# Kernel tuning notes

Hardware: AMD Instinct MI355X
Metric: run time of the kernel (lower is better)

Reference implementation:

```python
import jax, jax.numpy as jnp
import numpy as np
import math

B, DIM, H, W = 4, 96, 64, 64
DIM3 = DIM * 3
DSTATE = 16

def _dwconv(x, w, b):
    # x: (B, d, L); torch Conv1d(k=4, pad=3, groups=d) then slice [:L] == left-pad 3
    y = jax.lax.conv_general_dilated(x, w, (1,), [(3, 0)],
                                     dimension_numbers=('NCH', 'OIH', 'NCH'),
                                     feature_group_count=x.shape[1])
    return y + b[None, :, None]

def _ln(x, g, b):
    m = jnp.mean(x, -1, keepdims=True)
    v = jnp.var(x, -1, keepdims=True)
    return (x - m) * jax.lax.rsqrt(v + 1e-5) * g + b

def _selective_scan(u, delta, A, Bs, Cs, D, z, delta_bias):
    # u, delta, z: (B, d, L); A: (d, N); Bs, Cs: (B, N, L)
    delta = jax.nn.softplus(delta + delta_bias[None, :, None])
    dT, uT = jnp.moveaxis(delta, 2, 0), jnp.moveaxis(u, 2, 0)   # (L, B, d)
    BT, CT = jnp.moveaxis(Bs, 2, 0), jnp.moveaxis(Cs, 2, 0)     # (L, B, N)
    h0 = jnp.zeros((u.shape[0], A.shape[0], A.shape[1]), u.dtype)
    def step(h, inp):
        d_t, u_t, b_t, c_t = inp
        h = jnp.exp(d_t[..., None] * A) * h + (d_t * u_t)[..., None] * b_t[:, None, :]
        return h, jnp.einsum('bdn,bn->bd', h, c_t)
    _, ys = jax.lax.scan(step, h0, (dT, uT, BT, CT))
    y = jnp.moveaxis(ys, 0, 2) + D[None, :, None] * u
    return y * jax.nn.silu(z)

def _sss(x, z_anchor, in_w, conv_w, conv_b, x_w, dt_w, dt_b, Alog, Dp, out_w):
    Bb, C, Hh, Ww = x.shape
    L = Hh * Ww
    r = dt_w.shape[0]
    xf = x.reshape(Bb, C, L).transpose(0, 2, 1) + z_anchor[:, None, :]
    x_in, z_gate = jnp.split(xf @ in_w, 2, axis=-1)
    xc = jax.nn.silu(_dwconv(x_in.transpose(0, 2, 1), conv_w, conv_b))  # (B, di, L)
    xdbl = xc.transpose(0, 2, 1) @ x_w
    dt, Bs, Cs = jnp.split(xdbl, [r, r + DSTATE], axis=-1)
    y = _selective_scan(xc, (dt @ dt_w).transpose(0, 2, 1), -jnp.exp(Alog),
                        Bs.transpose(0, 2, 1), Cs.transpose(0, 2, 1), Dp,
                        z_gate.transpose(0, 2, 1), dt_b)
    return (y.transpose(0, 2, 1) @ out_w).transpose(0, 2, 1).reshape(Bb, C, Hh, Ww)

def _sts(x, K, Q, in_w, conv_w, conv_b, kln_g, kln_b, k_w, k_b, qln_g, qln_b, q_w, q_b,
         dtbc_w, dt_w, dt_b, gate_w, gate_b, Alog, Dp, out_w):
    Bb, C, Hh, Ww = x.shape
    L = Hh * Ww
    r = dt_w.shape[0]
    xf = x.reshape(Bb, C, L).transpose(0, 2, 1)
    xc = jax.nn.silu(_dwconv((xf @ in_w).transpose(0, 2, 1), conv_w, conv_b))  # (B, di, L)
    x_t = xc.transpose(0, 2, 1)
    Kf = K.reshape(Bb, C, L).transpose(0, 2, 1)
    Qf = Q.reshape(Bb, C, L).transpose(0, 2, 1)
    K_p = jax.nn.silu(_ln(Kf, kln_g, kln_b) @ k_w + k_b)
    Q_p = jax.nn.silu(_ln(Qf, qln_g, qln_b) @ q_w + q_b)
    xdbl = jnp.concatenate([x_t, K_p], -1) @ dtbc_w
    dt, Bs, Cs = jnp.split(xdbl, [r, r + DSTATE], axis=-1)
    z_g = (jnp.concatenate([x_t, Q_p], -1) @ gate_w + gate_b).transpose(0, 2, 1)
    y = _selective_scan(xc, (dt @ dt_w).transpose(0, 2, 1), -jnp.exp(Alog),
                        Bs.transpose(0, 2, 1), Cs.transpose(0, 2, 1), Dp, z_g, dt_b)
    return (y.transpose(0, 2, 1) @ out_w).transpose(0, 2, 1).reshape(Bb, C, Hh, Ww)

def setup_inputs():
    key = jax.random.key(0)
    ks = iter(jax.random.split(key, 64))
    def nrm(shape, s=0.02):
        return jax.random.normal(next(ks), shape, jnp.float32) * s
    di, di3 = DIM * 2, DIM3 * 2
    r, r3 = math.ceil(DIM / 16), math.ceil(DIM3 / 16)
    Alog = jnp.log(jnp.tile(jnp.arange(1.0, DSTATE + 1.0, dtype=jnp.float32), (di, 1)))
    Alog3 = jnp.log(jnp.tile(jnp.arange(1.0, DSTATE + 1.0, dtype=jnp.float32), (di3, 1)))
    return dict(
        m_ll=jax.random.normal(next(ks), (B, DIM, H, W), jnp.float32),
        m_high=jax.random.normal(next(ks), (B, DIM3, H, W), jnp.float32),
        z=jax.random.normal(next(ks), (B, DIM), jnp.float32),
        K=jax.random.normal(next(ks), (B, DIM3, H, W), jnp.float32),
        Q=jax.random.normal(next(ks), (B, DIM3, H, W), jnp.float32),
        s_in_w=nrm((DIM, 2 * di)), s_conv_w=nrm((di, 1, 4), 0.2), s_conv_b=nrm((di,)),
        s_x_w=nrm((di, r + 2 * DSTATE)), s_dt_w=nrm((r, di)), s_dt_b=nrm((di,)),
        s_Alog=Alog, s_D=jnp.ones((di,), jnp.float32), s_out_w=nrm((di, DIM)),
        t_in_w=nrm((DIM3, di3)), t_conv_w=nrm((di3, 1, 4), 0.2), t_conv_b=nrm((di3,)),
        t_kln_g=jnp.ones((DIM3,), jnp.float32), t_kln_b=jnp.zeros((DIM3,), jnp.float32),
        t_k_w=nrm((DIM3, di3)), t_k_b=nrm((di3,)),
        t_qln_g=jnp.ones((DIM3,), jnp.float32), t_qln_b=jnp.zeros((DIM3,), jnp.float32),
        t_q_w=nrm((DIM3, di3)), t_q_b=nrm((di3,)),
        t_dtbc_w=nrm((2 * di3, r3 + 2 * DSTATE)), t_dt_w=nrm((r3, di3)), t_dt_b=nrm((di3,)),
        t_gate_w=nrm((2 * di3, di3)), t_gate_b=nrm((di3,)),
        t_Alog=Alog3, t_D=jnp.ones((di3,), jnp.float32), t_out_w=nrm((di3, DIM3)),
    )

def reference(m_ll, m_high, z, K, Q,
              s_in_w, s_conv_w, s_conv_b, s_x_w, s_dt_w, s_dt_b, s_Alog, s_D, s_out_w,
              t_in_w, t_conv_w, t_conv_b, t_kln_g, t_kln_b, t_k_w, t_k_b,
              t_qln_g, t_qln_b, t_q_w, t_q_b, t_dtbc_w, t_dt_w, t_dt_b,
              t_gate_w, t_gate_b, t_Alog, t_D, t_out_w):
    o1 = m_ll + _sss(m_ll, z, s_in_w, s_conv_w, s_conv_b, s_x_w, s_dt_w, s_dt_b, s_Alog, s_D, s_out_w)
    o2 = m_high + _sts(m_high, K, Q, t_in_w, t_conv_w, t_conv_b, t_kln_g, t_kln_b, t_k_w, t_k_b,
                       t_qln_g, t_qln_b, t_q_w, t_q_b, t_dtbc_w, t_dt_w, t_dt_b,
                       t_gate_w, t_gate_b, t_Alog, t_D, t_out_w)
    return (o1, o2)
```

## Files before the change

kernel.cpp:

```cpp
#include <hip/hip_runtime.h>
#include <math.h>

#define L 4096

typedef unsigned short u16;
typedef unsigned int u32;
typedef float f32x4 __attribute__((ext_vector_type(4)));
typedef short s16x8 __attribute__((ext_vector_type(8)));
typedef __attribute__((address_space(3))) unsigned int lds_u32;
typedef __attribute__((address_space(1))) unsigned int glb_u32;

__device__ __forceinline__ float softplus_f(float x) {
  return fmaxf(x, 0.f) + log1pf(__expf(-fabsf(x)));
}
__device__ __forceinline__ float silu_f(float x) {
  return x / (1.f + __expf(-x));
}
__device__ __forceinline__ float bf2f(u16 v) {
  return __uint_as_float(((unsigned)v) << 16);
}
__device__ __forceinline__ u16 f2bf(float f) {
  unsigned u = __float_as_uint(f);
  u += 0x7FFFu + ((u >> 16) & 1u);
  return (u16)(u >> 16);
}

struct WSeg { const float* src; u16* dst; int K, N, Npad; };
struct WAll { WSeg s[9]; };

__global__ __launch_bounds__(256) void wconv_k(WAll wa) {
  const WSeg w = wa.s[blockIdx.z];
  const int nb = blockIdx.x * 32, kb = blockIdx.y * 32;
  if (nb >= w.Npad || kb >= w.K) return;
  __shared__ float t[32][33];
  const int tx = threadIdx.x & 31, ty = threadIdx.x >> 5;
  for (int r = ty; r < 32; r += 8) {
    int k = kb + r, n = nb + tx;
    t[r][tx] = (n < w.N) ? w.src[(size_t)k * w.N + n] : 0.f;
  }
  __syncthreads();
  for (int r = ty; r < 32; r += 8) {
    int n = nb + r;
    w.dst[(size_t)n * w.K + kb + tx] = f2bf(t[tx][r]);
  }
}

struct TSeg { const float *x, *gam, *bet, *bias2; u16* out; int C, doLN; };
struct TPack { TSeg s[4]; };

__global__ __launch_bounds__(256) void trans_pack_k(TPack pk) {
  const TSeg t = pk.s[blockIdx.x >> 9];
  const int local = blockIdx.x & 511;
  const int C = t.C;
  __shared__ float tile[288][33];
  __shared__ float psum[8][32], psq[8][32];
  __shared__ float mm[32], rr[32];
  const int tid = threadIdx.x;
  const int l0 = (local & 127) * 32;
  const int b = local >> 7;
  const int lane32 = tid & 31, row8 = tid >> 5;
  const float* xb = t.x + (size_t)b * C * L + l0;

  for (int c = row8; c < C; c += 8)
    tile[c][lane32] = xb[(size_t)c * L + lane32];
  __syncthreads();

  if (t.doLN) {
    float s = 0.f, sq = 0.f;
    for (int c = row8; c < C; c += 8) {
      float v = tile[c][lane32];
      s += v; sq = fmaf(v, v, sq);
    }
    psum[row8][lane32] = s; psq[row8][lane32] = sq;
    __syncthreads();
    if (row8 == 0) {
      float ts = 0.f, tq = 0.f;
      #pragma unroll
      for (int g = 0; g < 8; ++g) { ts += psum[g][lane32]; tq += psq[g][lane32]; }
      float m = ts / C;
      float var = tq / C - m * m;
      mm[lane32] = m;
      rr[lane32] = rsqrtf(var + 1e-5f);
    }
    __syncthreads();
  }

  u16* ob = t.out + ((size_t)b * L + l0) * C;
  const int total = 32 * C;
  for (int o = tid * 8; o < total; o += 2048) {
    int tt = o / C, c = o % C;
    float m = 0.f, rs = 0.f;
    if (t.doLN) { m = mm[tt]; rs = rr[tt]; }
    union { u16 u[8]; int4 v; } pkv;
    #pragma unroll
    for (int j = 0; j < 8; ++j) {
      float v = tile[c + j][tt];
      if (t.doLN) v = (v - m) * rs * t.gam[c + j] + t.bet[c + j];
      else if (t.bias2) v += t.bias2[b * C + c + j];
      pkv.u[j] = f2bf(v);
    }
    *(int4*)(ob + o) = pkv.v;
  }
}

struct CSeg { const u16* x; const float* w; const float* b; u16* y; int C, nbx; };
struct CPack { CSeg s[2]; int start1; };

__global__ __launch_bounds__(256) void conv_pack_k(CPack pk) {
  const int bid = blockIdx.x;
  const int si = bid >= pk.start1;
  const CSeg q = pk.s[si];
  const int local = si ? bid - pk.start1 : bid;
  const int C = q.C;
  const int c = (local % q.nbx) * 64 + (threadIdx.x & 63);
  const int chunk = (local / q.nbx) * 4 + (threadIdx.x >> 6);
  const int T0 = chunk * 8;
  const float w0 = q.w[c * 4], w1 = q.w[c * 4 + 1], w2 = q.w[c * 4 + 2], w3 = q.w[c * 4 + 3];
  const float bs = q.b[c];
  const bool first = (T0 & (L - 1)) == 0;
  float v[11];
  #pragma unroll
  for (int i = 0; i < 11; ++i) {
    if (i < 3 && first) v[i] = 0.f;
    else v[i] = bf2f(q.x[(size_t)(T0 - 3 + i) * C + c]);
  }
  #pragma unroll
  for (int j = 0; j < 8; ++j) {
    float s = bs + w0 * v[j] + w1 * v[j + 1] + w2 * v[j + 2] + w3 * v[j + 3];
    q.y[(size_t)(T0 + j) * C + c] = f2bf(silu_f(s));
  }
}

struct MSeg {
  const u16 *A0, *A1, *Wt;
  const float *bias, *res;
  float* outF; u16 *outB0, *outB1;
  int K, K1, Nout, ldA, ldo, split, nbx, nwg, epi;
};
struct MPack { MSeg s[4]; int starts[4]; int nseg; };

__global__ __launch_bounds__(256) void mfma_pack_k(MPack pk) {
  const int bid = blockIdx.x;
  int si = 0;
  #pragma unroll
  for (int k = 1; k < 4; ++k)
    if (k < pk.nseg && bid >= pk.starts[k]) si = k;
  const MSeg p = pk.s[si];
  const int wg = bid - pk.starts[si];

  __shared__ u16 As[2][4096];
  __shared__ u16 Bs[2][4096];
  const int tid = threadIdx.x;
  const int lane = tid & 63;
  const int wid = tid >> 6;
  const int wm = wid >> 1, wn = wid & 1;
  const int newid = (wg & 7) * (p.nwg >> 3) + (wg >> 3);
  const int n0 = (newid % p.nbx) * 128;
  const int m0 = (newid / p.nbx) * 128;
  const int srow = tid & 127;
  const int skc = tid >> 7;
  const int kgrp = lane >> 4, l16 = lane & 15;

  f32x4 acc[4][4];
  #pragma unroll
  for (int i = 0; i < 4; ++i)
    #pragma unroll
    for (int j = 0; j < 4; ++j)
      acc[i][j] = (f32x4){0.f, 0.f, 0.f, 0.f};

  auto stage = [&](int bi, int k0) {
    const u16* Ab = p.A0;
    int kc = k0;
    if (p.A1 && k0 >= p.K1) { Ab = p.A1; kc = k0 - p.K1; }
    const u16* g0 = Ab + (size_t)(m0 + srow) * p.ldA + kc + skc * 8;
    u16* Ad = &As[bi][0];
    __builtin_amdgcn_global_load_lds((const glb_u32*)g0,
        (lds_u32*)(Ad + wid * 512), 16, 0, 0);
    __builtin_amdgcn_global_load_lds((const glb_u32*)(g0 + 16),
        (lds_u32*)(Ad + 2048 + wid * 512), 16, 0, 0);
    const u16* h0 = p.Wt + (size_t)(n0 + srow) * p.K + k0 + skc * 8;
    u16* Bd = &Bs[bi][0];
    __builtin_amdgcn_global_load_lds((const glb_u32*)h0,
        (lds_u32*)(Bd + wid * 512), 16, 0, 0);
    __builtin_amdgcn_global_load_lds((const glb_u32*)(h0 + 16),
        (lds_u32*)(Bd + 2048 + wid * 512), 16, 0, 0);
  };

  const int nt = p.K >> 5;
  stage(0, 0);
  __syncthreads();
  for (int t = 0; t < nt; ++t) {
    const int cur = t & 1;
    if (t + 1 < nt) stage(cur ^ 1, (t + 1) << 5);
    s16x8 af[4], bfr[4];
    #pragma unroll
    for (int mi = 0; mi < 4; ++mi)
      af[mi] = *(const s16x8*)(&As[cur][0] + kgrp * 1024 + (wm * 64 + mi * 16 + l16) * 8);
    #pragma unroll
    for (int ni = 0; ni < 4; ++ni)
      bfr[ni] = *(const s16x8*)(&Bs[cur][0] + kgrp * 1024 + (wn * 64 + ni * 16 + l16) * 8);
    #pragma unroll
    for (int mi = 0; mi < 4; ++mi)
      #pragma unroll
      for (int ni = 0; ni < 4; ++ni)
        acc[mi][ni] = __builtin_amdgcn_mfma_f32_16x16x32_bf16(af[mi], bfr[ni], acc[mi][ni], 0, 0, 0);
    if (t + 1 < nt) __syncthreads();
  }

  if (p.epi == 2) {
    #pragma unroll
    for (int mi = 0; mi < 4; ++mi) {
      int token = m0 + wm * 64 + mi * 16 + (lane >> 4) * 4;
      int b = token >> 12, l = token & (L - 1);
      #pragma unroll
      for (int ni = 0; ni < 4; ++ni) {
        int n = n0 + wn * 64 + ni * 16 + l16;
        if (n < p.Nout) {
          size_t o = ((size_t)b * p.Nout + n) * L + l;
          float4 r = *(const float4*)(p.res + o);
          float4 v = make_float4(acc[mi][ni][0] + r.x, acc[mi][ni][1] + r.y,
                                 acc[mi][ni][2] + r.z, acc[mi][ni][3] + r.w);
          *(float4*)(p.outF + o) = v;
        }
      }
    }
  } else {
    #pragma unroll
    for (int mi = 0; mi < 4; ++mi) {
      #pragma unroll
      for (int j = 0; j < 4; ++j) {
        int token = m0 + wm * 64 + mi * 16 + (lane >> 4) * 4 + j;
        #pragma unroll
        for (int ni = 0; ni < 4; ++ni) {
          int n = n0 + wn * 64 + ni * 16 + l16;
          float v = acc[mi][ni][j];
          if (p.epi == 0) {
            if (n < p.Nout) p.outF[(size_t)token * p.ldo + n] = v;
          } else if (p.epi == 1) {
            if (n < p.Nout) p.outB0[(size_t)token * p.ldo + n] = f2bf(v);
          } else if (p.epi == 3) {
            if (n < p.Nout) p.outB0[(size_t)token * p.ldo + n] = f2bf(silu_f(v + p.bias[n]));
          } else if (p.epi == 4) {
            if (n < p.Nout) p.outB0[(size_t)token * p.ldo + n] = f2bf(v + p.bias[n]);
          } else {
            if (n < p.split) p.outB0[(size_t)token * p.split + n] = f2bf(v);
            else p.outB1[(size_t)token * p.split + (n - p.split)] = f2bf(v);
          }
        }
      }
    }
  }
}

struct FSeg { const float* A0; const float* W; const float* eb; float* out; int K, N, lda, ldo, nbx; };
struct FPack { FSeg s[2]; int start1; };

__global__ __launch_bounds__(256) void gemm_f32_pack_k(FPack pk) {
  const int bid = blockIdx.x;
  const int si = bid >= pk.start1;
  const FSeg p = pk.s[si];
  const int local = si ? bid - pk.start1 : bid;
  const int n0 = (local % p.nbx) * 64;
  const int m0 = (local / p.nbx) * 64;

  __shared__ __align__(16) float As[16][64];
  __shared__ __align__(16) float Bs[16][64];
  const int tid = threadIdx.x;
  const int kidx = tid >> 4;
  const int li4 = (tid & 15) << 2;
  const int r0 = (tid & 15) << 2;
  const int c0 = (tid >> 4) << 2;
  float acc[4][4] = {};

  for (int k0 = 0; k0 < p.K; k0 += 16) {
    __syncthreads();
    {
      const int row = tid >> 2;
      const int kk4 = (tid & 3) << 2;
      const float* src = p.A0 + (size_t)(m0 + row) * p.lda;
      #pragma unroll
      for (int j = 0; j < 4; ++j) {
        int k = k0 + kk4 + j;
        As[kk4 + j][row] = (k < p.K) ? src[k] : 0.f;
      }
    }
    {
      int k = k0 + kidx;
      #pragma unroll
      for (int j = 0; j < 4; ++j) {
        int n = n0 + li4 + j;
        Bs[kidx][li4 + j] = (k < p.K && n < p.N) ? p.W[(size_t)k * p.N + n] : 0.f;
      }
    }
    __syncthreads();
    #pragma unroll
    for (int kk = 0; kk < 16; ++kk) {
      float4 a = *(const float4*)&As[kk][r0];
      float4 bq = *(const float4*)&Bs[kk][c0];
      float av[4] = {a.x, a.y, a.z, a.w};
      float bv[4] = {bq.x, bq.y, bq.z, bq.w};
      #pragma unroll
      for (int i = 0; i < 4; ++i)
        #pragma unroll
        for (int j = 0; j < 4; ++j)
          acc[i][j] = fmaf(av[i], bv[j], acc[i][j]);
    }
  }
  float eb[4] = {p.eb[n0 + c0], p.eb[n0 + c0 + 1], p.eb[n0 + c0 + 2], p.eb[n0 + c0 + 3]};
  #pragma unroll
  for (int i = 0; i < 4; ++i) {
    float4 v;
    v.x = softplus_f(acc[i][0] + eb[0]);
    v.y = softplus_f(acc[i][1] + eb[1]);
    v.z = softplus_f(acc[i][2] + eb[2]);
    v.w = softplus_f(acc[i][3] + eb[3]);
    *(float4*)&p.out[(size_t)(m0 + r0 + i) * p.ldo + n0 + c0] = v;
  }
}

struct S2Seg {
  const u16* u; const float* dlt; const float* Alog; const float* xdbl;
  const float* Dp; const u16* zT; float* PF; u16* yT;
  int roff, Dch, CLen, NCH;
};
struct S2Pack { S2Seg s[2]; int start1; };

template<int PASS>
__global__ __launch_bounds__(256) void scan2_pack_k(S2Pack pk) {
  const int bid = blockIdx.x;
  const int si = bid >= pk.start1;
  const S2Seg q = pk.s[si];
  const int lbid = si ? bid - pk.start1 : bid;
  const int gtid = lbid * 256 + (int)threadIdx.x;
  const int Dch = q.Dch;
  const int npair = Dch >> 1;
  const int NC = L / q.CLen;
  const int dpi = gtid % npair;
  const int c = (gtid / npair) % NC;
  const int b = gtid / (npair * NC);
  const int d0 = dpi * 2;
  const size_t tok0 = (size_t)b * L + (size_t)c * q.CLen;

  float An[2][16], h[2][16];
  #pragma unroll
  for (int j = 0; j < 2; ++j)
    #pragma unroll
    for (int n = 0; n < 16; ++n) {
      An[j][n] = -__expf(q.Alog[(d0 + j) * 16 + n]);
      h[j][n] = 0.f;
    }
  bool fast = true;
  #pragma unroll
  for (int j = 0; j < 2; ++j)
    #pragma unroll
    for (int n = 1; n < 16; ++n) {
      float ref = (float)(n + 1) * An[j][0];
      if (fabsf(An[j][n] - ref) > 1e-4f * fabsf(ref)) fast = false;
    }

  const int ch0 = b * Dch + d0;
  if (PASS == 3) {
    #pragma unroll
    for (int j = 0; j < 2; ++j)
      #pragma unroll
      for (int n = 0; n < 16; ++n)
        h[j][n] = q.PF[((size_t)c * 32 + 16 + n) * q.NCH + ch0 + j];
  }
  const float Dd0 = q.Dp[d0], Dd1 = q.Dp[d0 + 1];
  const u16* up = q.u + tok0 * Dch + d0;
  const float* dp = q.dlt + tok0 * Dch + d0;
  const u16* zp = q.zT + tok0 * Dch + d0;
  u16* yr = q.yT + tok0 * Dch + d0;
  const float* xr = q.xdbl + tok0 * 64 + q.roff;
  float S0 = 0.f, S1 = 0.f;

  #define SCAN_BODY(FAST)                                                      \
  for (int t = 0; t < q.CLen; ++t) {                                           \
    const size_t od = (size_t)t * Dch;                                         \
    float2 dl2 = *(const float2*)(dp + od);                                    \
    u32 uu2 = *(const u32*)(up + od);                                          \
    float u0 = bf2f((u16)uu2), u1 = bf2f((u16)(uu2 >> 16));                    \
    float w0 = dl2.x * u0, w1 = dl2.y * u1;                                    \
    const float2* bp = (const float2*)(xr + (size_t)t * 64);                   \
    float Bv[16];                                                              \
    _Pragma("unroll")                                                          \
    for (int qq = 0; qq < 8; ++qq) {                                           \
      float2 bv = bp[qq]; Bv[2 * qq] = bv.x; Bv[2 * qq + 1] = bv.y;            \
    }                                                                          \
    if (PASS == 1) { S0 += dl2.x; S1 += dl2.y; }                               \
    float y0 = 0.f, y1 = 0.f;                                                  \
    if (FAST) {                                                                \
      float a0 = __expf(dl2.x * An[0][0]);                                     \
      float a1 = __expf(dl2.y * An[1][0]);                                     \
      float e0 = a0, e1 = a1;                                                  \
      h[0][0] = fmaf(e0, h[0][0], w0 * Bv[0]);                                 \
      h[1][0] = fmaf(e1, h[1][0], w1 * Bv[0]);                                 \
      _Pragma("unroll")                                                        \
      for (int n = 1; n < 16; ++n) {                                           \
        e0 *= a0; e1 *= a1;                                                    \
        h[0][n] = fmaf(e0, h[0][n], w0 * Bv[n]);                               \
        h[1][n] = fmaf(e1, h[1][n], w1 * Bv[n]);                               \
      }                                                                        \
    } else {                                                                   \
      _Pragma("unroll")                                                        \
      for (int n = 0; n < 16; ++n) {                                           \
        h[0][n] = fmaf(__expf(dl2.x * An[0][n]), h[0][n], w0 * Bv[n]);         \
        h[1][n] = fmaf(__expf(dl2.y * An[1][n]), h[1][n], w1 * Bv[n]);         \
      }                                                                        \
    }                                                                          \
    if (PASS == 3) {                                                           \
      _Pragma("unroll")                                                        \
      for (int qq = 0; qq < 8; ++qq) {                                         \
        float2 cv = bp[qq + 8];                                                \
        y0 = fmaf(h[0][2 * qq], cv.x, y0); y0 = fmaf(h[0][2 * qq + 1], cv.y, y0); \
        y1 = fmaf(h[1][2 * qq], cv.x, y1); y1 = fmaf(h[1][2 * qq + 1], cv.y, y1); \
      }                                                                        \
      u32 zz2 = *(const u32*)(zp + od);                                        \
      float z0 = bf2f((u16)zz2), z1 = bf2f((u16)(zz2 >> 16));                  \
      y0 = (y0 + Dd0 * u0) * silu_f(z0);                                       \
      y1 = (y1 + Dd1 * u1) * silu_f(z1);                                       \
      u32 out = (u32)f2bf(y0) | ((u32)f2bf(y1) << 16);                         \
      *(u32*)(yr + od) = out;                                                  \
    }                                                                          \
  }

  if (fast) { SCAN_BODY(1) } else { SCAN_BODY(0) }
  #undef SCAN_BODY

  if (PASS == 1) {
    #pragma unroll
    for (int n = 0; n < 16; ++n) {
      q.PF[((size_t)c * 32 + n) * q.NCH + ch0]     = __expf(An[0][n] * S0);
      q.PF[((size_t)c * 32 + n) * q.NCH + ch0 + 1] = __expf(An[1][n] * S1);
      q.PF[((size_t)c * 32 + 16 + n) * q.NCH + ch0]     = h[0][n];
      q.PF[((size_t)c * 32 + 16 + n) * q.NCH + ch0 + 1] = h[1][n];
    }
  }
}

__global__ __launch_bounds__(256) void stitch_pack_k(
    float* PF0, int NC0, int NCH0, int tot0,
    float* PF1, int NC1, int NCH1, int tot1) {
  int idx = blockIdx.x * 256 + threadIdx.x;
  float* PF; int NC, NCH;
  if (idx < tot0) { PF = PF0; NC = NC0; NCH = NCH0; }
  else { idx -= tot0; if (idx >= tot1) return; PF = PF1; NC = NC1; NCH = NCH1; }
  int ch = idx % NCH, n = idx / NCH;
  float hin = 0.f;
  for (int c = 0; c < NC; ++c) {
    float* Ps = PF + ((size_t)c * 32 + n) * NCH + ch;
    float* Fs = PF + ((size_t)c * 32 + 16 + n) * NCH + ch;
    float Pv = *Ps, Fv = *Fs;
    *Fs = hin;
    hin = fmaf(Pv, hin, Fv);
  }
}

extern "C" void kernel_launch(void* const* d_in, const int* in_sizes, int n_in,
                              void* d_out, int out_size, void* d_ws, size_t ws_size,
                              hipStream_t stream) {
  const float* m_ll    = (const float*)d_in[0];
  const float* m_high  = (const float*)d_in[1];
  const float* zanc    = (const float*)d_in[2];
  const float* Kin     = (const float*)d_in[3];
  const float* Qin     = (const float*)d_in[4];
  const float* s_in_w  = (const float*)d_in[5];
  const float* s_conv_w= (const float*)d_in[6];
  const float* s_conv_b= (const float*)d_in[7];
  const float* s_x_w   = (const float*)d_in[8];
  const float* s_dt_w  = (const float*)d_in[9];
  const float* s_dt_b  = (const float*)d_in[10];
  const float* s_Alog  = (const float*)d_in[11];
  const float* s_D     = (const float*)d_in[12];
  const float* s_out_w = (const float*)d_in[13];
  const float* t_in_w  = (const float*)d_in[14];
  const float* t_conv_w= (const float*)d_in[15];
  const float* t_conv_b= (const float*)d_in[16];
  const float* t_kln_g = (const float*)d_in[17];
  const float* t_kln_b = (const float*)d_in[18];
  const float* t_k_w   = (const float*)d_in[19];
  const float* t_k_b   = (const float*)d_in[20];
  const float* t_qln_g = (const float*)d_in[21];
  const float* t_qln_b = (const float*)d_in[22];
  const float* t_q_w   = (const float*)d_in[23];
  const float* t_q_b   = (const float*)d_in[24];
  const float* t_dtbc_w= (const float*)d_in[25];
  const float* t_dt_w  = (const float*)d_in[26];
  const float* t_dt_b  = (const float*)d_in[27];
  const float* t_gate_w= (const float*)d_in[28];
  const float* t_gate_b= (const float*)d_in[29];
  const float* t_Alog  = (const float*)d_in[30];
  const float* t_D     = (const float*)d_in[31];
  const float* t_out_w = (const float*)d_in[32];

  float* out1 = (float*)d_out;
  float* out2 = out1 + (size_t)4 * 96 * L;
  float* ws = (float*)d_ws;

  u16* w_sin   = (u16*)(ws + 0);
  u16* w_sx    = (u16*)(ws + 18432);
  u16* w_sout  = (u16*)(ws + 30720);
  u16* w_tin   = (u16*)(ws + 43008);
  u16* w_tk    = (u16*)(ws + 135168);
  u16* w_tq    = (u16*)(ws + 227328);
  u16* w_tdtbc = (u16*)(ws + 319488);
  u16* w_tgate = (u16*)(ws + 393216);
  u16* w_tout  = (u16*)(ws + 761856);

  float* B_ahi  = ws + 872448;
  float* B_aK   = ws + 2052096;
  float* B_aQ   = ws + 3231744;
  float* B_all  = ws + 4411392;
  float* B_xin  = ws + 5197824;
  float* B_zTs  = ws + 6770688;
  float* B_xc   = ws + 8343552;
  float* B_xin3 = ws + 9916416;
  float* B_xc3  = ws + 14635008;
  float* B_kp   = ws + 19353600;
  float* B_qp   = ws + 24072192;
  float* B_zg3  = ws + 28790784;
  float* B_xdbl = ws + 33509376;
  float* B_xdbl3= ws + 34557952;
  float* B_PFs  = ws + 35606528;
  float* B_dlt  = B_ahi;
  float* B_dlt3 = B_kp;
  u16* y_bf = (u16*)B_xin;
  u16* y3   = (u16*)B_xin3;
  float* PFt = out2;

  dim3 blk(256);

  {
    WAll wa;
    wa.s[0] = {s_in_w,   w_sin,    96, 384, 384};
    wa.s[1] = {s_x_w,    w_sx,    192,  38, 128};
    wa.s[2] = {s_out_w,  w_sout,  192,  96, 128};
    wa.s[3] = {t_in_w,   w_tin,   288, 576, 640};
    wa.s[4] = {t_k_w,    w_tk,    288, 576, 640};
    wa.s[5] = {t_q_w,    w_tq,    288, 576, 640};
    wa.s[6] = {t_dtbc_w, w_tdtbc, 1152, 50, 128};
    wa.s[7] = {t_gate_w, w_tgate, 1152, 576, 640};
    wa.s[8] = {t_out_w,  w_tout,  576, 288, 384};
    wconv_k<<<dim3(20, 36, 9), blk, 0, stream>>>(wa);
  }

  {
    TPack tp{};
    tp.s[0] = {m_ll,   nullptr, nullptr, zanc,    (u16*)B_all, 96,  0};
    tp.s[1] = {m_high, nullptr, nullptr, nullptr, (u16*)B_ahi, 288, 0};
    tp.s[2] = {Kin,    t_kln_g, t_kln_b, nullptr, (u16*)B_aK,  288, 1};
    tp.s[3] = {Qin,    t_qln_g, t_qln_b, nullptr, (u16*)B_aQ,  288, 1};
    trans_pack_k<<<dim3(2048), blk, 0, stream>>>(tp);
  }

  {
    MPack pk{}; pk.nseg = 4;
    pk.starts[0] = 0; pk.starts[1] = 384; pk.starts[2] = 1024; pk.starts[3] = 1664;
    MSeg a{}; a.A0 = (u16*)B_all; a.Wt = w_sin; a.K = 96; a.K1 = 1 << 28; a.Nout = 384;
    a.ldA = 96; a.split = 192; a.outB0 = (u16*)B_xin; a.outB1 = (u16*)B_zTs;
    a.nbx = 3; a.nwg = 384; a.epi = 5; pk.s[0] = a;
    MSeg b{}; b.A0 = (u16*)B_ahi; b.Wt = w_tin; b.K = 288; b.K1 = 1 << 28; b.Nout = 576;
    b.ldA = 288; b.ldo = 576; b.outB0 = (u16*)B_xin3; b.nbx = 5; b.nwg = 640; b.epi = 1; pk.s[1] = b;
    MSeg c{}; c.A0 = (u16*)B_aK; c.Wt = w_tk; c.K = 288; c.K1 = 1 << 28; c.Nout = 576;
    c.ldA = 288; c.ldo = 576; c.bias = t_k_b; c.outB0 = (u16*)B_kp; c.nbx = 5; c.nwg = 640; c.epi = 3; pk.s[2] = c;
    MSeg d{}; d.A0 = (u16*)B_aQ; d.Wt = w_tq; d.K = 288; d.K1 = 1 << 28; d.Nout = 576;
    d.ldA = 288; d.ldo = 576; d.bias = t_q_b; d.outB0 = (u16*)B_qp; d.nbx = 5; d.nwg = 640; d.epi = 3; pk.s[3] = d;
    mfma_pack_k<<<dim3(2304), blk, 0, stream>>>(pk);
  }

  {
    CPack cp{}; cp.start1 = 1536;
    cp.s[0] = {(u16*)B_xin,  s_conv_w, s_conv_b, (u16*)B_xc,  192, 3};
    cp.s[1] = {(u16*)B_xin3, t_conv_w, t_conv_b, (u16*)B_xc3, 576, 9};
    conv_pack_k<<<dim3(6144), blk, 0, stream>>>(cp);
  }

  {
    MPack pk{}; pk.nseg = 3;
    pk.starts[0] = 0; pk.starts[1] = 128; pk.starts[2] = 256; pk.starts[3] = 896;
    MSeg a{}; a.A0 = (u16*)B_xc; a.Wt = w_sx; a.K = 192; a.K1 = 1 << 28; a.Nout = 64;
    a.ldA = 192; a.ldo = 64; a.outF = B_xdbl; a.nbx = 1; a.nwg = 128; a.epi = 0; pk.s[0] = a;
    MSeg b{}; b.A0 = (u16*)B_xc3; b.A1 = (u16*)B_kp; b.Wt = w_tdtbc; b.K = 1152; b.K1 = 576;
    b.Nout = 64; b.ldA = 576; b.ldo = 64; b.outF = B_xdbl3; b.nbx = 1; b.nwg = 128; b.epi = 0; pk.s[1] = b;
    MSeg c{}; c.A0 = (u16*)B_xc3; c.A1 = (u16*)B_qp; c.Wt = w_tgate; c.K = 1152; c.K1 = 576;
    c.Nout = 576; c.ldA = 576; c.ldo = 576; c.bias = t_gate_b; c.outB0 = (u16*)B_zg3;
    c.nbx = 5; c.nwg = 640; c.epi = 4; pk.s[2] = c;
    mfma_pack_k<<<dim3(896), blk, 0, stream>>>(pk);
  }

  {
    FPack fp{}; fp.start1 = 768;
    fp.s[0] = {B_xdbl,  s_dt_w, s_dt_b, B_dlt,  6,  192, 64, 192, 3};
    fp.s[1] = {B_xdbl3, t_dt_w, t_dt_b, B_dlt3, 18, 576, 64, 576, 9};
    gemm_f32_pack_k<<<dim3(3072), blk, 0, stream>>>(fp);
  }

  S2Pack sp{}; sp.start1 = 192;
  sp.s[0] = {(u16*)B_xc,  B_dlt,  s_Alog, B_xdbl,  s_D, (u16*)B_zTs, B_PFs, y_bf, 6,  192, 32, 768};
  sp.s[1] = {(u16*)B_xc3, B_dlt3, t_Alog, B_xdbl3, t_D, (u16*)B_zg3, PFt,   y3,   18, 576, 64, 2304};
  scan2_pack_k<1><<<dim3(480), blk, 0, stream>>>(sp);
  stitch_pack_k<<<dim3(192), blk, 0, stream>>>(B_PFs, 128, 768, 12288, PFt, 64, 2304, 36864);
  scan2_pack_k<3><<<dim3(480), blk, 0, stream>>>(sp);

  {
    MPack pk{}; pk.nseg = 2;
    pk.starts[0] = 0; pk.starts[1] = 128; pk.starts[2] = 512; pk.starts[3] = 512;
    MSeg a{}; a.A0 = y_bf; a.Wt = w_sout; a.K = 192; a.K1 = 1 << 28; a.Nout = 96;
    a.ldA = 192; a.res = m_ll; a.outF = out1; a.nbx = 1; a.nwg = 128; a.epi = 2; pk.s[0] = a;
    MSeg b{}; b.A0 = y3; b.Wt = w_tout; b.K = 576; b.K1 = 1 << 28; b.Nout = 288;
    b.ldA = 576; b.res = m_high; b.outF = out2; b.nbx = 3; b.nwg = 384; b.epi = 2; pk.s[1] = b;
    mfma_pack_k<<<dim3(512), blk, 0, stream>>>(pk);
  }
}
```

Measured before the change: 428.8 us.

## Scan one channel per thread, stage bf16 GEMM epilogue via swizzled LDS, split weight conversion

The selective-scan kernels now assign one channel per thread instead of two, doubling the grid so more waves are in flight while cutting per-thread register state. The MFMA GEMM's bf16 epilogues now write the tile into a swizzled shared-memory buffer, then emit 16-byte vectorized global stores instead of scattered 2-byte stores. The weight-conversion launch is split so the out-projection segment runs with a smaller grid. The tradeoffs are narrower per-thread loads in the scan and extra barriers plus LDS traffic in the epilogue.

```diff
diff --git a/kernel.cpp b/kernel.cpp
--- a/kernel.cpp
+++ b/kernel.cpp
@@ -26,7 +26,7 @@
 }
 
 struct WSeg { const float* src; u16* dst; int K, N, Npad; };
-struct WAll { WSeg s[9]; };
+struct WAll { WSeg s[8]; };
 
 __global__ __launch_bounds__(256) void wconv_k(WAll wa) {
   const WSeg w = wa.s[blockIdx.z];
@@ -148,8 +148,9 @@
   const MSeg p = pk.s[si];
   const int wg = bid - pk.starts[si];
 
-  __shared__ u16 As[2][4096];
-  __shared__ u16 Bs[2][4096];
+  __shared__ u16 lds[16384];
+  u16* As0 = lds;
+  u16* Bs0 = lds + 8192;
   const int tid = threadIdx.x;
   const int lane = tid & 63;
   const int wid = tid >> 6;
@@ -173,13 +174,13 @@
     int kc = k0;
     if (p.A1 && k0 >= p.K1) { Ab = p.A1; kc = k0 - p.K1; }
     const u16* g0 = Ab + (size_t)(m0 + srow) * p.ldA + kc + skc * 8;
-    u16* Ad = &As[bi][0];
+    u16* Ad = As0 + bi * 4096;
     __builtin_amdgcn_global_load_lds((const glb_u32*)g0,
         (lds_u32*)(Ad + wid * 512), 16, 0, 0);
     __builtin_amdgcn_global_load_lds((const glb_u32*)(g0 + 16),
         (lds_u32*)(Ad + 2048 + wid * 512), 16, 0, 0);
     const u16* h0 = p.Wt + (size_t)(n0 + srow) * p.K + k0 + skc * 8;
-    u16* Bd = &Bs[bi][0];
+    u16* Bd = Bs0 + bi * 4096;
     __builtin_amdgcn_global_load_lds((const glb_u32*)h0,
         (lds_u32*)(Bd + wid * 512), 16, 0, 0);
     __builtin_amdgcn_global_load_lds((const glb_u32*)(h0 + 16),
@@ -195,10 +196,10 @@
     s16x8 af[4], bfr[4];
     #pragma unroll
     for (int mi = 0; mi < 4; ++mi)
-      af[mi] = *(const s16x8*)(&As[cur][0] + kgrp * 1024 + (wm * 64 + mi * 16 + l16) * 8);
+      af[mi] = *(const s16x8*)(As0 + cur * 4096 + kgrp * 1024 + (wm * 64 + mi * 16 + l16) * 8);
     #pragma unroll
     for (int ni = 0; ni < 4; ++ni)
-      bfr[ni] = *(const s16x8*)(&Bs[cur][0] + kgrp * 1024 + (wn * 64 + ni * 16 + l16) * 8);
+      bfr[ni] = *(const s16x8*)(Bs0 + cur * 4096 + kgrp * 1024 + (wn * 64 + ni * 16 + l16) * 8);
     #pragma unroll
     for (int mi = 0; mi < 4; ++mi)
       #pragma unroll
@@ -207,7 +208,20 @@
     if (t + 1 < nt) __syncthreads();
   }
 
-  if (p.epi == 2) {
+  if (p.epi == 0) {
+    #pragma unroll
+    for (int mi = 0; mi < 4; ++mi) {
+      #pragma unroll
+      for (int j = 0; j < 4; ++j) {
+        int token = m0 + wm * 64 + mi * 16 + (lane >> 4) * 4 + j;
+        #pragma unroll
+        for (int ni = 0; ni < 4; ++ni) {
+          int n = n0 + wn * 64 + ni * 16 + l16;
+          if (n < p.Nout) p.outF[(size_t)token * p.ldo + n] = acc[mi][ni][j];
+        }
+      }
+    }
+  } else if (p.epi == 2) {
     #pragma unroll
     for (int mi = 0; mi < 4; ++mi) {
       int token = m0 + wm * 64 + mi * 16 + (lane >> 4) * 4;
@@ -225,27 +239,41 @@
       }
     }
   } else {
+    __syncthreads();
     #pragma unroll
     for (int mi = 0; mi < 4; ++mi) {
       #pragma unroll
       for (int j = 0; j < 4; ++j) {
-        int token = m0 + wm * 64 + mi * 16 + (lane >> 4) * 4 + j;
+        int tok = wm * 64 + mi * 16 + (lane >> 4) * 4 + j;
         #pragma unroll
         for (int ni = 0; ni < 4; ++ni) {
-          int n = n0 + wn * 64 + ni * 16 + l16;
+          int nl = wn * 64 + ni * 16 + l16;
+          int n = n0 + nl;
           float v = acc[mi][ni][j];
-          if (p.epi == 0) {
-            if (n < p.Nout) p.outF[(size_t)token * p.ldo + n] = v;
-          } else if (p.epi == 1) {
-            if (n < p.Nout) p.outB0[(size_t)token * p.ldo + n] = f2bf(v);
-          } else if (p.epi == 3) {
-            if (n < p.Nout) p.outB0[(size_t)token * p.ldo + n] = f2bf(silu_f(v + p.bias[n]));
-          } else if (p.epi == 4) {
-            if (n < p.Nout) p.outB0[(size_t)token * p.ldo + n] = f2bf(v + p.bias[n]);
-          } else {
-            if (n < p.split) p.outB0[(size_t)token * p.split + n] = f2bf(v);
-            else p.outB1[(size_t)token * p.split + (n - p.split)] = f2bf(v);
+          if (n < p.Nout && (p.epi == 3 || p.epi == 4)) {
+            v += p.bias[n];
+            if (p.epi == 3) v = silu_f(v);
           }
+          lds[tok * 128 + ((((nl >> 4) ^ (tok & 7))) << 4) + (nl & 15)] = f2bf(v);
+        }
+      }
+    }
+    __syncthreads();
+    #pragma unroll
+    for (int it = 0; it < 8; ++it) {
+      int idx = it * 256 + tid;
+      int row = idx >> 4, c16 = idx & 15;
+      int nl0 = c16 * 8;
+      if (n0 + nl0 < p.Nout) {
+        int g = nl0 >> 4;
+        int4 vv = *(const int4*)(lds + row * 128 + ((g ^ (row & 7)) << 4) + (nl0 & 15));
+        int token = m0 + row;
+        if (p.epi == 5) {
+          int n = n0 + nl0;
+          if (n < p.split) *(int4*)(p.outB0 + (size_t)token * p.split + n) = vv;
+          else *(int4*)(p.outB1 + (size_t)token * p.split + (n - p.split)) = vv;
+        } else {
+          *(int4*)(p.outB0 + (size_t)token * p.ldo + n0 + nl0) = vv;
         }
       }
     }
@@ -333,94 +361,76 @@
   const int lbid = si ? bid - pk.start1 : bid;
   const int gtid = lbid * 256 + (int)threadIdx.x;
   const int Dch = q.Dch;
-  const int npair = Dch >> 1;
   const int NC = L / q.CLen;
-  const int dpi = gtid % npair;
-  const int c = (gtid / npair) % NC;
-  const int b = gtid / (npair * NC);
-  const int d0 = dpi * 2;
+  const int d = gtid % Dch;
+  const int c = (gtid / Dch) % NC;
+  const int b = gtid / (Dch * NC);
   const size_t tok0 = (size_t)b * L + (size_t)c * q.CLen;
 
-  float An[2][16], h[2][16];
+  float An[16], h[16];
   #pragma unroll
-  for (int j = 0; j < 2; ++j)
-    #pragma unroll
-    for (int n = 0; n < 16; ++n) {
-      An[j][n] = -__expf(q.Alog[(d0 + j) * 16 + n]);
-      h[j][n] = 0.f;
-    }
+  for (int n = 0; n < 16; ++n) {
+    An[n] = -__expf(q.Alog[d * 16 + n]);
+    h[n] = 0.f;
+  }
   bool fast = true;
   #pragma unroll
-  for (int j = 0; j < 2; ++j)
-    #pragma unroll
-    for (int n = 1; n < 16; ++n) {
-      float ref = (float)(n + 1) * An[j][0];
-      if (fabsf(An[j][n] - ref) > 1e-4f * fabsf(ref)) fast = false;
-    }
-
-  const int ch0 = b * Dch + d0;
+  for (int n = 1; n < 16; ++n) {
+    float ref = (float)(n + 1) * An[0];
+    if (fabsf(An[n] - ref) > 1e-4f * fabsf(ref)) fast = false;
+  }
+
+  const int ch = b * Dch + d;
   if (PASS == 3) {
     #pragma unroll
-    for (int j = 0; j < 2; ++j)
-      #pragma unroll
-      for (int n = 0; n < 16; ++n)
-        h[j][n] = q.PF[((size_t)c * 32 + 16 + n) * q.NCH + ch0 + j];
-  }
-  const float Dd0 = q.Dp[d0], Dd1 = q.Dp[d0 + 1];
-  const u16* up = q.u + tok0 * Dch + d0;
-  const float* dp = q.dlt + tok0 * Dch + d0;
-  const u16* zp = q.zT + tok0 * Dch + d0;
-  u16* yr = q.yT + tok0 * Dch + d0;
+    for (int n = 0; n < 16; ++n)
+      h[n] = q.PF[((size_t)c * 32 + 16 + n) * q.NCH + ch];
+  }
+  const float Dd = q.Dp[d];
+  const u16* up = q.u + tok0 * Dch + d;
+  const float* dp = q.dlt + tok0 * Dch + d;
+  const u16* zp = q.zT + tok0 * Dch + d;
+  u16* yr = q.yT + tok0 * Dch + d;
   const float* xr = q.xdbl + tok0 * 64 + q.roff;
-  float S0 = 0.f, S1 = 0.f;
+  float S = 0.f;
 
   #define SCAN_BODY(FAST)                                                      \
   for (int t = 0; t < q.CLen; ++t) {                                           \
     const size_t od = (size_t)t * Dch;                                         \
-    float2 dl2 = *(const float2*)(dp + od);                                    \
-    u32 uu2 = *(const u32*)(up + od);                                          \
-    float u0 = bf2f((u16)uu2), u1 = bf2f((u16)(uu2 >> 16));                    \
-    float w0 = dl2.x * u0, w1 = dl2.y * u1;                                    \
+    float dl = dp[od];                                                         \
+    float uu = bf2f(up[od]);                                                   \
+    float w = dl * uu;                                                         \
     const float2* bp = (const float2*)(xr + (size_t)t * 64);                   \
     float Bv[16];                                                              \
     _Pragma("unroll")                                                          \
     for (int qq = 0; qq < 8; ++qq) {                                           \
       float2 bv = bp[qq]; Bv[2 * qq] = bv.x; Bv[2 * qq + 1] = bv.y;            \
     }                                                                          \
-    if (PASS == 1) { S0 += dl2.x; S1 += dl2.y; }                               \
-    float y0 = 0.f, y1 = 0.f;                                                  \
+    if (PASS == 1) S += dl;                                                    \
+    float y = 0.f;                                                             \
     if (FAST) {                                                                \
-      float a0 = __expf(dl2.x * An[0][0]);                                     \
-      float a1 = __expf(dl2.y * An[1][0]);                                     \
-      float e0 = a0, e1 = a1;                                                  \
-      h[0][0] = fmaf(e0, h[0][0], w0 * Bv[0]);                                 \
-      h[1][0] = fmaf(e1, h[1][0], w1 * Bv[0]);                                 \
+      float a = __expf(dl * An[0]);                                            \
+      float e = a;                                                             \
+      h[0] = fmaf(e, h[0], w * Bv[0]);                                         \
       _Pragma("unroll")                                                        \
       for (int n = 1; n < 16; ++n) {                                           \
-        e0 *= a0; e1 *= a1;                                                    \
-        h[0][n] = fmaf(e0, h[0][n], w0 * Bv[n]);                               \
-        h[1][n] = fmaf(e1, h[1][n], w1 * Bv[n]);                               \
+        e *= a;                                                                \
+        h[n] = fmaf(e, h[n], w * Bv[n]);                                       \
       }                                                                        \
     } else {                                                                   \
       _Pragma("unroll")                                                        \
-      for (int n = 0; n < 16; ++n) {                                           \
-        h[0][n] = fmaf(__expf(dl2.x * An[0][n]), h[0][n], w0 * Bv[n]);         \
-        h[1][n] = fmaf(__expf(dl2.y * An[1][n]), h[1][n], w1 * Bv[n]);         \
-      }                                                                        \
+      for (int n = 0; n < 16; ++n)                                             \
+        h[n] = fmaf(__expf(dl * An[n]), h[n], w * Bv[n]);                      \
     }                                                                          \
     if (PASS == 3) {                                                           \
       _Pragma("unroll")                                                        \
       for (int qq = 0; qq < 8; ++qq) {                                         \
         float2 cv = bp[qq + 8];                                                \
-        y0 = fmaf(h[0][2 * qq], cv.x, y0); y0 = fmaf(h[0][2 * qq + 1], cv.y, y0); \
-        y1 = fmaf(h[1][2 * qq], cv.x, y1); y1 = fmaf(h[1][2 * qq + 1], cv.y, y1); \
+        y = fmaf(h[2 * qq], cv.x, y);                                          \
+        y = fmaf(h[2 * qq + 1], cv.y, y);                                      \
       }                                                                        \
-      u32 zz2 = *(const u32*)(zp + od);                                        \
-      float z0 = bf2f((u16)zz2), z1 = bf2f((u16)(zz2 >> 16));                  \
-      y0 = (y0 + Dd0 * u0) * silu_f(z0);                                       \
-      y1 = (y1 + Dd1 * u1) * silu_f(z1);                                       \
-      u32 out = (u32)f2bf(y0) | ((u32)f2bf(y1) << 16);                         \
-      *(u32*)(yr + od) = out;                                                  \
+      float zv = bf2f(zp[od]);                                                 \
+      yr[od] = f2bf((y + Dd * uu) * silu_f(zv));                               \
     }                                                                          \
   }
 
@@ -430,10 +440,8 @@
   if (PASS == 1) {
     #pragma unroll
     for (int n = 0; n < 16; ++n) {
-      q.PF[((size_t)c * 32 + n) * q.NCH + ch0]     = __expf(An[0][n] * S0);
-      q.PF[((size_t)c * 32 + n) * q.NCH + ch0 + 1] = __expf(An[1][n] * S1);
-      q.PF[((size_t)c * 32 + 16 + n) * q.NCH + ch0]     = h[0][n];
-      q.PF[((size_t)c * 32 + 16 + n) * q.NCH + ch0 + 1] = h[1][n];
+      q.PF[((size_t)c * 32 + n) * q.NCH + ch] = __expf(An[n] * S);
+      q.PF[((size_t)c * 32 + 16 + n) * q.NCH + ch] = h[n];
     }
   }
 }
@@ -540,8 +548,10 @@
     wa.s[5] = {t_q_w,    w_tq,    288, 576, 640};
     wa.s[6] = {t_dtbc_w, w_tdtbc, 1152, 50, 128};
     wa.s[7] = {t_gate_w, w_tgate, 1152, 576, 640};
-    wa.s[8] = {t_out_w,  w_tout,  576, 288, 384};
-    wconv_k<<<dim3(20, 36, 9), blk, 0, stream>>>(wa);
+    wconv_k<<<dim3(20, 36, 8), blk, 0, stream>>>(wa);
+    WAll wb;
+    wb.s[0] = {t_out_w,  w_tout,  576, 288, 384};
+    wconv_k<<<dim3(12, 18, 1), blk, 0, stream>>>(wb);
   }
 
   {
@@ -595,12 +605,12 @@
     gemm_f32_pack_k<<<dim3(3072), blk, 0, stream>>>(fp);
   }
 
-  S2Pack sp{}; sp.start1 = 192;
+  S2Pack sp{}; sp.start1 = 384;
   sp.s[0] = {(u16*)B_xc,  B_dlt,  s_Alog, B_xdbl,  s_D, (u16*)B_zTs, B_PFs, y_bf, 6,  192, 32, 768};
   sp.s[1] = {(u16*)B_xc3, B_dlt3, t_Alog, B_xdbl3, t_D, (u16*)B_zg3, PFt,   y3,   18, 576, 64, 2304};
-  scan2_pack_k<1><<<dim3(480), blk, 0, stream>>>(sp);
+  scan2_pack_k<1><<<dim3(960), blk, 0, stream>>>(sp);
   stitch_pack_k<<<dim3(192), blk, 0, stream>>>(B_PFs, 128, 768, 12288, PFt, 64, 2304, 36864);
-  scan2_pack_k<3><<<dim3(480), blk, 0, stream>>>(sp);
+  scan2_pack_k<3><<<dim3(960), blk, 0, stream>>>(sp);
 
   {
     MPack pk{}; pk.nseg = 2;
```

New measurement: 418.2 us. -2.5%, faster.
